# Optimization experiments

Hardware: AMD Instinct MI355X
Metric: run time of the kernel (lower is better)

The kernel has to match this reference:

```python
import jax, jax.numpy as jnp
import numpy as np

# ---- config (matches init_kwargs) ----
B, NP, DIM, HEADS, DH, NDIM = 32, 576, 512, 8, 64, 16
N = NP + 1                 # seq len incl cls token = 577
INNER = HEADS * DH         # 512


def setup_inputs() -> dict:
    key = jax.random.key(0)
    ks = jax.random.split(key, 11)
    D2 = 2 * DIM  # bidirectional EMA doubles kernel dim
    return {
        "x": jax.random.normal(ks[0], (B, N, DIM), jnp.float32),
        "W_qk": jax.random.normal(ks[1], (DIM, 2 * INNER), jnp.float32) / np.float32(np.sqrt(DIM)),
        "W_v": jax.random.normal(ks[2], (DIM, INNER), jnp.float32) / np.float32(np.sqrt(DIM)),
        "W_out": jax.random.normal(ks[3], (INNER, DIM), jnp.float32) / np.float32(np.sqrt(INNER)),
        "b_out": jnp.zeros((DIM,), jnp.float32),
        "rel_bias": jax.random.normal(ks[4], (2 * N - 1,), jnp.float32) * 0.02,
        "ema_delta": jax.random.normal(ks[5], (D2, NDIM, 1), jnp.float32),
        "ema_alpha": jax.random.normal(ks[6], (D2, NDIM, 1), jnp.float32),
        "ema_beta": jax.random.normal(ks[7], (D2, NDIM, 1), jnp.float32) * 0.5,
        "ema_gamma": jax.random.normal(ks[8], (D2, NDIM), jnp.float32) * 0.5,
        "ema_omega": jax.random.normal(ks[9], (DIM,), jnp.float32),
    }


def _ema_move(x, delta, alpha, beta, gamma, omega):
    """Bidirectional MultiHeadEMA (MEGA) via FFT convolution. x: (B, L, D)."""
    b, L, d = x.shape
    scale = jnp.asarray(np.sqrt(1.0 / NDIM), x.dtype)
    p = jax.nn.sigmoid(delta)                      # (2D, N, 1)
    q = 1.0 - p * jax.nn.sigmoid(alpha)            # (2D, N, 1), in (0,1)
    vander = jnp.arange(L, dtype=x.dtype)[None, None, :] * jnp.log(q)  # (2D, N, L)
    kern = (p * beta) * jnp.exp(vander)            # (2D, N, L)
    k = jnp.einsum('dnl,dn->dl', kern, gamma * scale)  # (2D, L)
    k1, k2 = k[:d], k[d:]
    # combined bidirectional kernel, length 2L-1
    kk = jnp.pad(k1, ((0, 0), (L - 1, 0))) + jnp.pad(k2[:, ::-1], ((0, 0), (0, L - 1)))
    xt = jnp.pad(x.transpose(0, 2, 1), ((0, 0), (0, 0), (L - 1, 0)))  # (B, D, 2L-1)
    fft_len = 2 * L - 1
    nfft = 2 * fft_len
    out = jnp.fft.irfft(jnp.fft.rfft(xt, n=nfft) * jnp.fft.rfft(kk, n=nfft)[None], n=nfft)
    s = 2 * L - 2
    out = out[..., s:s + L].transpose(0, 2, 1).astype(x.dtype)  # (B, L, D)
    return jax.nn.silu(out + x * omega)


def _rel_pos_bias(rb, seq_len):
    """RelativePositionalBias (MEGA): (2*N-1,) param -> (seq_len, seq_len) bias."""
    max_pos = N
    bvec = rb[max_pos - seq_len: max_pos + seq_len - 1]   # (2*seq_len-1,)
    t = jnp.pad(bvec, (0, seq_len))
    t = jnp.tile(t, seq_len)[:-seq_len].reshape(seq_len, 3 * seq_len - 2)
    r = (2 * seq_len - 1) // 2
    return t[:, r:t.shape[1] - r]


def reference(x, W_qk, W_v, W_out, b_out, rel_bias,
              ema_delta, ema_alpha, ema_beta, ema_gamma, ema_omega):
    b, n, _ = x.shape
    cls_tok = x[:, :1]
    moved = _ema_move(x[:, 1:], ema_delta, ema_alpha, ema_beta, ema_gamma, ema_omega)
    xm = jnp.concatenate([cls_tok, moved], axis=1)        # (B, N, DIM)
    q, k = jnp.split(xm @ W_qk, 2, axis=-1)
    v = xm @ W_v                                          # smooth_v_as_well=True

    def heads(t):
        return t.reshape(b, n, HEADS, DH).transpose(0, 2, 1, 3)  # (B, H, N, DH)

    q, k, v = heads(q), heads(k), heads(v)
    dots = jnp.einsum('bhid,bhjd->bhij', q, k) * (DH ** -0.5)
    attn = jax.nn.softmax(dots, axis=-1)
    attn = attn + _rel_pos_bias(rel_bias, n)[None, None]  # bias added AFTER softmax
    out = jnp.einsum('bhij,bhjd->bhid', attn, v)
    out = out.transpose(0, 2, 1, 3).reshape(b, n, INNER)
    return out @ W_out + b_out
```

## Files before the change

### kernel.cpp

```cpp
#include <hip/hip_runtime.h>

typedef unsigned short ushort;

typedef __bf16 bf16x8 __attribute__((ext_vector_type(8)));
typedef float  f32x4  __attribute__((ext_vector_type(4)));
typedef unsigned short u16x8 __attribute__((ext_vector_type(8)));
typedef unsigned short u16x4 __attribute__((ext_vector_type(4)));
typedef unsigned int   u32x2 __attribute__((ext_vector_type(2)));

static constexpr int BB   = 32;
static constexpr int NN   = 577;
static constexpr int LL   = 576;
static constexpr int DIMC = 512;
static constexpr int BN   = BB * NN;

static constexpr size_t SZ_WQKVT = 1536ull * 512 * 2;
static constexpr size_t SZ_WOUTT = 512ull * 512 * 2;
static constexpr size_t SZ_QK    = (size_t)BN * 1024 * 2;
static constexpr size_t SZ_V     = (size_t)BN * 512 * 2;
static constexpr size_t SZ_VT    = 256ull * 64 * 640 * 2;
static constexpr size_t OFF_WQKVT = 0;
static constexpr size_t OFF_WOUTT = OFF_WQKVT + SZ_WQKVT;
static constexpr size_t OFF_QTAB  = OFF_WOUTT + SZ_WOUTT;
static constexpr size_t OFF_CTAB  = OFF_QTAB + 65536;
static constexpr size_t OFF_QK    = OFF_CTAB + 65536;
static constexpr size_t OFF_V     = OFF_QK + SZ_QK;
static constexpr size_t OFF_REGION= OFF_V + SZ_V;
static constexpr size_t OFF_XM    = OFF_REGION;
static constexpr size_t OFF_VT    = OFF_REGION;
static constexpr size_t OFF_AO    = OFF_REGION + SZ_VT;
static constexpr size_t WS_NEEDED = OFF_AO + SZ_V;

__device__ __forceinline__ ushort bf16bits(float f) {
  unsigned int u = __builtin_bit_cast(unsigned int, f);
  u = (u + 0x7fffu + ((u >> 16) & 1u)) >> 16;
  return (ushort)u;
}
__device__ __forceinline__ float sigmoidf_(float z) { return 1.f / (1.f + __expf(-z)); }
__device__ __forceinline__ float siluf(float z)     { return z / (1.f + __expf(-z)); }

__global__ __launch_bounds__(256) void k_prep(
    const float* __restrict__ delta, const float* __restrict__ alpha,
    const float* __restrict__ beta,  const float* __restrict__ gamma,
    const float* __restrict__ Wqk,   const float* __restrict__ Wv,
    const float* __restrict__ Wout,
    float* __restrict__ qtab, float* __restrict__ ctab,
    ushort* __restrict__ Wqkvt, ushort* __restrict__ Woutt)
{
  int idx = blockIdx.x * 256 + threadIdx.x;
  if (idx < 16384) {
    float p = sigmoidf_(delta[idx]);
    float q = 1.f - p * sigmoidf_(alpha[idx]);
    qtab[idx] = q;
    ctab[idx] = p * beta[idx] * gamma[idx] * 0.25f;
  }
  int i2 = idx - 16384;
  if (i2 >= 0 && i2 < 1536 * 512) {
    int n = i2 >> 9, k = i2 & 511;
    float w = (n < 1024) ? Wqk[k * 1024 + n] : Wv[k * 512 + (n - 1024)];
    Wqkvt[i2] = bf16bits(w);
  }
  int i3 = i2 - 1536 * 512;
  if (i3 >= 0 && i3 < 512 * 512) {
    int n = i3 >> 9, k = i3 & 511;
    Woutt[i3] = bf16bits(Wout[k * 512 + n]);
  }
}

__global__ __launch_bounds__(64) void k_ema_scan(
    const float* __restrict__ x, const float* __restrict__ qtab,
    const float* __restrict__ ctab, float* __restrict__ y1, float* __restrict__ y2)
{
  const int bx = blockIdx.x;
  const int b  = blockIdx.y;
  if (bx < 8) {
    const int d = bx * 64 + threadIdx.x;
    float q[16], c[16], h[16];
    #pragma unroll
    for (int n = 0; n < 16; ++n) { q[n] = qtab[d*16+n]; c[n] = ctab[d*16+n]; h[n] = 0.f; }
    const float* xp = x  + ((size_t)b * NN + 1) * DIMC + d;
    float*       yp = y1 + ((size_t)b * LL)     * DIMC + d;
    float xn[8];
    #pragma unroll
    for (int u = 0; u < 8; ++u) xn[u] = xp[u * DIMC];
    for (int blk = 0; blk < 72; ++blk) {
      float xv[8];
      #pragma unroll
      for (int u = 0; u < 8; ++u) xv[u] = xn[u];
      if (blk < 71) {
        #pragma unroll
        for (int u = 0; u < 8; ++u) xn[u] = xp[((blk + 1) * 8 + u) * DIMC];
      }
      #pragma unroll
      for (int u = 0; u < 8; ++u) {
        float xx = xv[u], y = 0.f;
        #pragma unroll
        for (int n = 0; n < 16; ++n) { h[n] = fmaf(q[n], h[n], xx); y = fmaf(c[n], h[n], y); }
        yp[(blk * 8 + u) * DIMC] = y;
      }
    }
  } else {
    const int d = (bx - 8) * 64 + threadIdx.x;
    float q[16], c[16], g[16];
    #pragma unroll
    for (int n = 0; n < 16; ++n) { q[n] = qtab[(d+512)*16+n]; c[n] = ctab[(d+512)*16+n]; g[n] = 0.f; }
    const float* xp = x  + ((size_t)b * NN + 1) * DIMC + d;
    float*       yp = y2 + ((size_t)b * LL)     * DIMC + d;
    float xn[8];
    #pragma unroll
    for (int u = 0; u < 8; ++u) xn[u] = xp[(568 + u) * DIMC];
    for (int blk = 71; blk >= 0; --blk) {
      float xv[8];
      #pragma unroll
      for (int u = 0; u < 8; ++u) xv[u] = xn[u];
      if (blk > 0) {
        #pragma unroll
        for (int u = 0; u < 8; ++u) xn[u] = xp[((blk - 1) * 8 + u) * DIMC];
      }
      #pragma unroll
      for (int u = 7; u >= 0; --u) {
        float xx = xv[u], y = 0.f;
        #pragma unroll
        for (int n = 0; n < 16; ++n) { g[n] = fmaf(q[n], g[n], xx); y = fmaf(c[n], g[n], y); }
        yp[(blk * 8 + u) * DIMC] = y;
      }
    }
  }
}

__global__ __launch_bounds__(256) void k_ema_comb(
    const float* __restrict__ x, const float* __restrict__ y1,
    const float* __restrict__ y2, const float* __restrict__ omega,
    ushort* __restrict__ xm)
{
  size_t v = (size_t)blockIdx.x * 256 + threadIdx.x;
  size_t e = v * 4;
  int n = (int)(e >> 9);
  int d = (int)(e & 511);
  int b = n / 577;
  int i = n - b * 577;
  f32x4 xv = *(const f32x4*)(x + e);
  u16x4 o;
  if (i == 0) {
    #pragma unroll
    for (int k = 0; k < 4; ++k) o[k] = bf16bits(xv[k]);
  } else {
    size_t ey = ((size_t)b * LL + (i - 1)) * DIMC + d;
    f32x4 a  = *(const f32x4*)(y1 + ey);
    f32x4 c2 = *(const f32x4*)(y2 + ey);
    f32x4 om = *(const f32x4*)(omega + d);
    #pragma unroll
    for (int k = 0; k < 4; ++k) o[k] = bf16bits(siluf(a[k] + c2[k] + xv[k] * om[k]));
  }
  *(u16x4*)(xm + e) = o;
}

__global__ __launch_bounds__(256) void k_qkv(
    const ushort* __restrict__ A, const ushort* __restrict__ Bt,
    ushort* __restrict__ qk, ushort* __restrict__ v)
{
  __shared__ alignas(16) ushort lA[128 * 40];
  __shared__ alignas(16) ushort lB[128 * 40];
  const int tid = threadIdx.x, wv = tid >> 6, lane = tid & 63;
  const int quad = lane >> 4, c16 = lane & 15;
  const int fid = blockIdx.y * 12 + blockIdx.x;
  const int xcd = fid & 7, ord = fid >> 3;
  const int wg  = (xcd < 4 ? xcd * 218 : 872 + (xcd - 4) * 217) + ord;
  const int row0 = (wg / 12) * 128, n0 = (wg % 12) * 128;
  const int wm = (wv >> 1) * 64, wn = (wv & 1) * 64;
  f32x4 z4 = {0.f, 0.f, 0.f, 0.f};
  f32x4 acc[4][4];
  #pragma unroll
  for (int mi = 0; mi < 4; ++mi)
    #pragma unroll
    for (int ni = 0; ni < 4; ++ni) acc[mi][ni] = z4;

  for (int kt = 0; kt < 16; ++kt) {
    const int k0 = kt * 32;
    u16x8 sa[2], sb[2];
    #pragma unroll
    for (int it = 0; it < 2; ++it) {
      int ch = it * 256 + tid;
      int r = ch >> 2, cc = ch & 3;
      int grow = row0 + r; if (grow > BN - 1) grow = BN - 1;
      sa[it] = *(const u16x8*)(A + (size_t)grow * 512 + k0 + cc * 8);
      sb[it] = *(const u16x8*)(Bt + (size_t)(n0 + r) * 512 + k0 + cc * 8);
    }
    __syncthreads();
    #pragma unroll
    for (int it = 0; it < 2; ++it) {
      int ch = it * 256 + tid;
      int r = ch >> 2, cc = ch & 3;
      *(u16x8*)(lA + r * 40 + cc * 8) = sa[it];
      *(u16x8*)(lB + r * 40 + cc * 8) = sb[it];
    }
    __syncthreads();
    bf16x8 af[4], bfv[4];
    #pragma unroll
    for (int mi = 0; mi < 4; ++mi)
      af[mi] = *(const bf16x8*)(lA + (wm + mi * 16 + c16) * 40 + quad * 8);
    #pragma unroll
    for (int ni = 0; ni < 4; ++ni)
      bfv[ni] = *(const bf16x8*)(lB + (wn + ni * 16 + c16) * 40 + quad * 8);
    #pragma unroll
    for (int mi = 0; mi < 4; ++mi)
      #pragma unroll
      for (int ni = 0; ni < 4; ++ni)
        acc[mi][ni] = __builtin_amdgcn_mfma_f32_16x16x32_bf16(af[mi], bfv[ni], acc[mi][ni], 0, 0, 0);
  }
  const bool isv = (n0 >= 1024);
  const float osc = (n0 < 512) ? 0.125f : 1.0f;
  #pragma unroll
  for (int mi = 0; mi < 4; ++mi) {
    #pragma unroll
    for (int r = 0; r < 4; ++r) {
      int grow = row0 + wm + mi * 16 + quad * 4 + r;
      if (grow < BN) {
        #pragma unroll
        for (int ni = 0; ni < 4; ++ni) {
          int col = n0 + wn + ni * 16 + c16;
          ushort vb = bf16bits(acc[mi][ni][r] * osc);
          if (!isv) qk[(size_t)grow * 1024 + col] = vb;
          else      v[(size_t)grow * 512 + (col - 1024)] = vb;
        }
      }
    }
  }
}

__global__ __launch_bounds__(256) void k_vtrans(
    const ushort* __restrict__ v, ushort* __restrict__ vt)
{
  __shared__ alignas(16) ushort lt[64 * 72];
  const int tid = threadIdx.x;
  const int bh = blockIdx.y, b = bh >> 3, h = bh & 7;
  const int j0 = blockIdx.x * 64;
  #pragma unroll
  for (int pass = 0; pass < 2; ++pass) {
    int cch = pass * 256 + tid;
    int jl = cch >> 3, cc = cch & 7;
    int gj = j0 + jl;
    u16x8 val = {0, 0, 0, 0, 0, 0, 0, 0};
    if (gj < 577) val = *(const u16x8*)(v + ((size_t)(b * NN + gj)) * 512 + h * 64 + cc * 8);
    *(u16x8*)(lt + jl * 72 + cc * 8) = val;
  }
  __syncthreads();
  #pragma unroll
  for (int pass = 0; pass < 2; ++pass) {
    int cch = pass * 256 + tid;
    int dh = cch >> 3, jc = cch & 7;
    u16x8 o;
    #pragma unroll
    for (int e = 0; e < 8; ++e) o[e] = lt[(jc * 8 + e) * 72 + dh];
    *(u16x8*)(vt + ((size_t)(bh * 64 + dh)) * 640 + j0 + jc * 8) = o;
  }
}

__global__ __launch_bounds__(256) void k_fattn(
    const ushort* __restrict__ qk, const ushort* __restrict__ vt,
    const float* __restrict__ relb, ushort* __restrict__ ao)
{
  __shared__ alignas(16) ushort lk[64 * 64];
  __shared__ alignas(16) ushort lv[64 * 64];
  __shared__ alignas(16) ushort lp[128 * 64];
  __shared__ ushort lbias16[1280];
  const int tid = threadIdx.x, wv = tid >> 6, lane = tid & 63;
  const int quad = lane >> 4, c16 = lane & 15;
  const int bh = blockIdx.x, b = bh >> 3, h = bh & 7;
  const int i0 = blockIdx.y * 128, wm = wv * 32;
  for (int t = tid; t < 1280; t += 256) {
    int idx = t - 64;
    lbias16[t] = (idx >= 0 && idx < 1153) ? bf16bits(relb[idx]) : (ushort)0;
  }
  bf16x8 aq[2][2];
  #pragma unroll
  for (int ms = 0; ms < 2; ++ms) {
    int gi = i0 + wm + ms * 16 + c16; if (gi > 576) gi = 576;
    const ushort* qp = qk + ((size_t)(b * NN + gi)) * 1024 + h * 64;
    #pragma unroll
    for (int kk = 0; kk < 2; ++kk)
      aq[ms][kk] = *(const bf16x8*)(qp + (kk * 4 + quad) * 8);
  }
  const int s_r = tid >> 3, s_c = tid & 7;
  const ushort* kbase = qk + ((size_t)b * NN) * 1024 + 512 + h * 64 + s_c * 8;
  const ushort* vbase = vt + ((size_t)bh * 64) * 640 + s_c * 8;

  float lsum[2] = {0.f, 0.f};
  f32x4 z4 = {0.f, 0.f, 0.f, 0.f};
  f32x4 accp[2][4], accb[2][4];
  #pragma unroll
  for (int ms = 0; ms < 2; ++ms)
    #pragma unroll
    for (int ns = 0; ns < 4; ++ns) { accp[ms][ns] = z4; accb[ms][ns] = z4; }

  u16x8 sk[2], sv[2];
  #pragma unroll
  for (int it = 0; it < 2; ++it) {
    int r = it * 32 + s_r;
    sk[it] = *(const u16x8*)(kbase + (size_t)r * 1024);
    sv[it] = *(const u16x8*)(vbase + (size_t)r * 640);
  }

  for (int jt = 0; jt < 10; ++jt) {
    __syncthreads();
    #pragma unroll
    for (int it = 0; it < 2; ++it) {
      int r = it * 32 + s_r;
      int pc = (s_c ^ (r & 7)) * 8;
      *(u16x8*)(lk + r * 64 + pc) = sk[it];
      *(u16x8*)(lv + r * 64 + pc) = sv[it];
    }
    __syncthreads();
    #pragma unroll
    for (int ms = 0; ms < 2; ++ms) {
      f32x4 dacc[4] = {z4, z4, z4, z4};
      #pragma unroll
      for (int kk = 0; kk < 2; ++kk) {
        const int ck = kk * 4 + quad;
        #pragma unroll
        for (int ns = 0; ns < 4; ++ns) {
          const int row = ns * 16 + c16;
          bf16x8 bk = *(const bf16x8*)(lk + row * 64 + ((ck ^ (row & 7)) * 8));
          dacc[ns] = __builtin_amdgcn_mfma_f32_16x16x32_bf16(bk, aq[ms][kk], dacc[ns], 0, 0, 0);
        }
      }
      const int irow = wm + ms * 16 + c16;
      const int xr = irow & 7;
      #pragma unroll
      for (int ns = 0; ns < 4; ++ns) {
        float ex[4];
        #pragma unroll
        for (int r = 0; r < 4; ++r) {
          float e = __expf(dacc[ns][r]);
          if (jt == 9 && (ns * 16 + quad * 4 + r) >= 1) e = 0.f;
          ex[r] = e;
        }
        lsum[ms] += (ex[0] + ex[1]) + (ex[2] + ex[3]);
        unsigned int p0 = (unsigned int)bf16bits(ex[0]) | ((unsigned int)bf16bits(ex[1]) << 16);
        unsigned int p1 = (unsigned int)bf16bits(ex[2]) | ((unsigned int)bf16bits(ex[3]) << 16);
        u32x2 pw = {p0, p1};
        const int lc = ns * 2 + (quad >> 1);
        *(u32x2*)(lp + irow * 64 + ((lc ^ xr) * 8) + (quad & 1) * 4) = pw;
      }
    }
    __syncthreads();
    if (jt < 9) {
      const int j0n = (jt + 1) * 64;
      #pragma unroll
      for (int it = 0; it < 2; ++it) {
        int r = it * 32 + s_r;
        int gj = j0n + r; if (gj > 576) gj = 576;
        sk[it] = *(const u16x8*)(kbase + (size_t)gj * 1024);
        sv[it] = *(const u16x8*)(vbase + (size_t)r * 640 + j0n);
      }
    }
    const int j0 = jt * 64;
    #pragma unroll
    for (int kk = 0; kk < 2; ++kk) {
      const int ck = kk * 4 + quad;
      bf16x8 ap[2], ab[2];
      #pragma unroll
      for (int ms = 0; ms < 2; ++ms) {
        const int row = wm + ms * 16 + c16;
        ap[ms] = *(const bf16x8*)(lp + row * 64 + ((ck ^ (row & 7)) * 8));
        u16x8 abu;
        const int base = 64 + 576 + j0 + kk * 32 + quad * 8 - (i0 + row);
        #pragma unroll
        for (int e = 0; e < 8; ++e) abu[e] = lbias16[base + e];
        ab[ms] = __builtin_bit_cast(bf16x8, abu);
      }
      #pragma unroll
      for (int ns = 0; ns < 4; ++ns) {
        const int row = ns * 16 + c16;
        bf16x8 bV = *(const bf16x8*)(lv + row * 64 + ((ck ^ (row & 7)) * 8));
        #pragma unroll
        for (int ms = 0; ms < 2; ++ms) {
          accp[ms][ns] = __builtin_amdgcn_mfma_f32_16x16x32_bf16(ap[ms], bV, accp[ms][ns], 0, 0, 0);
          accb[ms][ns] = __builtin_amdgcn_mfma_f32_16x16x32_bf16(ab[ms], bV, accb[ms][ns], 0, 0, 0);
        }
      }
    }
  }
  float tot[2];
  #pragma unroll
  for (int ms = 0; ms < 2; ++ms) {
    float t = lsum[ms];
    t += __shfl_xor(t, 16);
    t += __shfl_xor(t, 32);
    tot[ms] = t;
  }
  #pragma unroll
  for (int ms = 0; ms < 2; ++ms) {
    #pragma unroll
    for (int r = 0; r < 4; ++r) {
      float li = 1.f / __shfl(tot[ms], quad * 4 + r);
      int ii = i0 + wm + ms * 16 + quad * 4 + r;
      if (ii < 577) {
        #pragma unroll
        for (int ns = 0; ns < 4; ++ns)
          ao[((size_t)(b * NN + ii)) * 512 + h * 64 + ns * 16 + c16] =
              bf16bits(accp[ms][ns][r] * li + accb[ms][ns][r]);
      }
    }
  }
}

__global__ __launch_bounds__(256) void k_out(
    const ushort* __restrict__ A, const ushort* __restrict__ Bt,
    const float* __restrict__ bout, float* __restrict__ out)
{
  __shared__ alignas(16) ushort lA[128 * 40];
  __shared__ alignas(16) ushort lB[128 * 40];
  const int tid = threadIdx.x, wv = tid >> 6, lane = tid & 63;
  const int quad = lane >> 4, c16 = lane & 15;
  const int row0 = blockIdx.y * 128, n0 = blockIdx.x * 128;
  const int wm = (wv >> 1) * 64, wn = (wv & 1) * 64;
  f32x4 z4 = {0.f, 0.f, 0.f, 0.f};
  f32x4 acc[4][4];
  #pragma unroll
  for (int mi = 0; mi < 4; ++mi)
    #pragma unroll
    for (int ni = 0; ni < 4; ++ni) acc[mi][ni] = z4;

  for (int kt = 0; kt < 16; ++kt) {
    const int k0 = kt * 32;
    u16x8 sa[2], sb[2];
    #pragma unroll
    for (int it = 0; it < 2; ++it) {
      int ch = it * 256 + tid;
      int r = ch >> 2, cc = ch & 3;
      int grow = row0 + r; if (grow > BN - 1) grow = BN - 1;
      sa[it] = *(const u16x8*)(A + (size_t)grow * 512 + k0 + cc * 8);
      sb[it] = *(const u16x8*)(Bt + (size_t)(n0 + r) * 512 + k0 + cc * 8);
    }
    __syncthreads();
    #pragma unroll
    for (int it = 0; it < 2; ++it) {
      int ch = it * 256 + tid;
      int r = ch >> 2, cc = ch & 3;
      *(u16x8*)(lA + r * 40 + cc * 8) = sa[it];
      *(u16x8*)(lB + r * 40 + cc * 8) = sb[it];
    }
    __syncthreads();
    bf16x8 af[4], bfv[4];
    #pragma unroll
    for (int mi = 0; mi < 4; ++mi)
      af[mi] = *(const bf16x8*)(lA + (wm + mi * 16 + c16) * 40 + quad * 8);
    #pragma unroll
    for (int ni = 0; ni < 4; ++ni)
      bfv[ni] = *(const bf16x8*)(lB + (wn + ni * 16 + c16) * 40 + quad * 8);
    #pragma unroll
    for (int mi = 0; mi < 4; ++mi)
      #pragma unroll
      for (int ni = 0; ni < 4; ++ni)
        acc[mi][ni] = __builtin_amdgcn_mfma_f32_16x16x32_bf16(af[mi], bfv[ni], acc[mi][ni], 0, 0, 0);
  }
  #pragma unroll
  for (int mi = 0; mi < 4; ++mi) {
    #pragma unroll
    for (int r = 0; r < 4; ++r) {
      int grow = row0 + wm + mi * 16 + quad * 4 + r;
      if (grow < BN) {
        #pragma unroll
        for (int ni = 0; ni < 4; ++ni) {
          int col = n0 + wn + ni * 16 + c16;
          out[(size_t)grow * 512 + col] = acc[mi][ni][r] + bout[col];
        }
      }
    }
  }
}

extern "C" void kernel_launch(void* const* d_in, const int* in_sizes, int n_in,
                              void* d_out, int out_size, void* d_ws, size_t ws_size,
                              hipStream_t stream) {
  (void)in_sizes; (void)n_in; (void)out_size;
  if (ws_size < WS_NEEDED) return;
  const float* x    = (const float*)d_in[0];
  const float* Wqk  = (const float*)d_in[1];
  const float* Wv   = (const float*)d_in[2];
  const float* Wout = (const float*)d_in[3];
  const float* bout = (const float*)d_in[4];
  const float* relb = (const float*)d_in[5];
  const float* edel = (const float*)d_in[6];
  const float* ealp = (const float*)d_in[7];
  const float* ebet = (const float*)d_in[8];
  const float* egam = (const float*)d_in[9];
  const float* eome = (const float*)d_in[10];

  char* ws = (char*)d_ws;
  ushort* Wqkvt = (ushort*)(ws + OFF_WQKVT);
  ushort* Woutt = (ushort*)(ws + OFF_WOUTT);
  float*  qtab  = (float*)(ws + OFF_QTAB);
  float*  ctab  = (float*)(ws + OFF_CTAB);
  ushort* qkb   = (ushort*)(ws + OFF_QK);
  ushort* vb    = (ushort*)(ws + OFF_V);
  ushort* xm    = (ushort*)(ws + OFF_XM);
  ushort* vtb   = (ushort*)(ws + OFF_VT);
  ushort* aob   = (ushort*)(ws + OFF_AO);
  float*  outp  = (float*)d_out;
  float*  y1    = outp;
  float*  y2    = (float*)(ws + OFF_QK);

  k_prep<<<dim3(4160), dim3(256), 0, stream>>>(edel, ealp, ebet, egam, Wqk, Wv, Wout,
                                               qtab, ctab, Wqkvt, Woutt);
  k_ema_scan<<<dim3(16, 32), dim3(64), 0, stream>>>(x, qtab, ctab, y1, y2);
  k_ema_comb<<<dim3(9232), dim3(256), 0, stream>>>(x, y1, y2, eome, xm);
  k_qkv<<<dim3(12, 145), dim3(256), 0, stream>>>(xm, Wqkvt, qkb, vb);
  k_vtrans<<<dim3(10, 256), dim3(256), 0, stream>>>(vb, vtb);
  k_fattn<<<dim3(256, 5), dim3(256), 0, stream>>>(qkb, vtb, relb, aob);
  k_out<<<dim3(4, 145), dim3(256), 0, stream>>>(aob, Woutt, bout, outp);
}
```

Measured before the change: 356.8 us.

## Split EMA recurrence into chunked three-phase parallel scan

Replaces the single sequential EMA scan kernel (512 blocks of 64 threads, each walking 576 steps) with a three-phase chunked scan. The first phase computes per-chunk end states over 7 chunks of 72 steps, the middle kernel propagates carries across chunks using q^72, and the third phase reruns each chunk from its carried-in state and emits outputs. This raises parallelism 8x so more of the GPU is busy, at the cost of two extra launches, re-reading x and extra state traffic. Chunk states are stored in the attention-output workspace region.

```diff
diff --git a/kernel.cpp b/kernel.cpp
--- a/kernel.cpp
+++ b/kernel.cpp
@@ -29,6 +29,7 @@
 static constexpr size_t OFF_XM    = OFF_REGION;
 static constexpr size_t OFF_VT    = OFF_REGION;
 static constexpr size_t OFF_AO    = OFF_REGION + SZ_VT;
+static constexpr size_t OFF_ST    = OFF_AO;
 static constexpr size_t WS_NEEDED = OFF_AO + SZ_V;
 
 __device__ __forceinline__ ushort bf16bits(float f) {
@@ -67,27 +68,117 @@
   }
 }
 
-__global__ __launch_bounds__(64) void k_ema_scan(
+
+__global__ __launch_bounds__(64) void k_ema_p1(
     const float* __restrict__ x, const float* __restrict__ qtab,
-    const float* __restrict__ ctab, float* __restrict__ y1, float* __restrict__ y2)
-{
-  const int bx = blockIdx.x;
-  const int b  = blockIdx.y;
-  if (bx < 8) {
-    const int d = bx * 64 + threadIdx.x;
+    float* __restrict__ st)
+{
+  const int gx = blockIdx.x, cy = blockIdx.y, b = blockIdx.z;
+  if (gx < 8) {
+    const int d = gx * 64 + threadIdx.x;
+    float q[16], h[16];
+    #pragma unroll
+    for (int n = 0; n < 16; ++n) { q[n] = qtab[d*16+n]; h[n] = 0.f; }
+    const float* xp = x + ((size_t)b * NN + 1) * DIMC + d;
+    const int blo = cy * 9;
+    float xn[8];
+    #pragma unroll
+    for (int u = 0; u < 8; ++u) xn[u] = xp[(blo * 8 + u) * DIMC];
+    for (int blk = blo; blk < blo + 9; ++blk) {
+      float xv[8];
+      #pragma unroll
+      for (int u = 0; u < 8; ++u) xv[u] = xn[u];
+      if (blk < blo + 8) {
+        #pragma unroll
+        for (int u = 0; u < 8; ++u) xn[u] = xp[((blk + 1) * 8 + u) * DIMC];
+      }
+      #pragma unroll
+      for (int u = 0; u < 8; ++u) {
+        float xx = xv[u];
+        #pragma unroll
+        for (int n = 0; n < 16; ++n) h[n] = fmaf(q[n], h[n], xx);
+      }
+    }
+    float* sp = st + (((size_t)b * 8 + cy) * 16) * 512 + d;
+    #pragma unroll
+    for (int n = 0; n < 16; ++n) sp[n * 512] = h[n];
+  } else {
+    const int d = (gx - 8) * 64 + threadIdx.x;
+    float q[16], g[16];
+    #pragma unroll
+    for (int n = 0; n < 16; ++n) { q[n] = qtab[(d+512)*16+n]; g[n] = 0.f; }
+    const float* xp = x + ((size_t)b * NN + 1) * DIMC + d;
+    const int blo = (7 - cy) * 9;
+    float xn[8];
+    #pragma unroll
+    for (int u = 0; u < 8; ++u) xn[u] = xp[((blo + 8) * 8 + u) * DIMC];
+    for (int blk = blo + 8; blk >= blo; --blk) {
+      float xv[8];
+      #pragma unroll
+      for (int u = 0; u < 8; ++u) xv[u] = xn[u];
+      if (blk > blo) {
+        #pragma unroll
+        for (int u = 0; u < 8; ++u) xn[u] = xp[((blk - 1) * 8 + u) * DIMC];
+      }
+      #pragma unroll
+      for (int u = 7; u >= 0; --u) {
+        float xx = xv[u];
+        #pragma unroll
+        for (int n = 0; n < 16; ++n) g[n] = fmaf(q[n], g[n], xx);
+      }
+    }
+    float* sp = st + (((size_t)(32 + b) * 8 + cy) * 16) * 512 + d;
+    #pragma unroll
+    for (int n = 0; n < 16; ++n) sp[n * 512] = g[n];
+  }
+}
+
+__global__ __launch_bounds__(256) void k_ema_mid(
+    const float* __restrict__ qtab, float* __restrict__ st)
+{
+  int idx = blockIdx.x * 256 + threadIdx.x;
+  int d = idx & 511;
+  int rest = idx >> 9;
+  int n = rest & 15;
+  int db = rest >> 4;
+  int dir = db >> 5;
+  float q = qtab[(((size_t)dir << 9) + d) * 16 + n];
+  float q2 = q * q, q4 = q2 * q2, q8 = q4 * q4;
+  float q16 = q8 * q8, q32 = q16 * q16, q64 = q32 * q32;
+  float qL = q64 * q8;
+  float h = 0.f;
+  float* sp = st + ((size_t)db * 128 + n) * 512 + d;
+  #pragma unroll
+  for (int c = 0; c < 8; ++c) {
+    float tmp = (c < 7) ? sp[c * 8192] : 0.f;
+    sp[c * 8192] = h;
+    h = fmaf(qL, h, tmp);
+  }
+}
+
+__global__ __launch_bounds__(64) void k_ema_p3(
+    const float* __restrict__ x, const float* __restrict__ qtab,
+    const float* __restrict__ ctab, const float* __restrict__ st,
+    float* __restrict__ y1, float* __restrict__ y2)
+{
+  const int gx = blockIdx.x, cy = blockIdx.y, b = blockIdx.z;
+  if (gx < 8) {
+    const int d = gx * 64 + threadIdx.x;
     float q[16], c[16], h[16];
-    #pragma unroll
-    for (int n = 0; n < 16; ++n) { q[n] = qtab[d*16+n]; c[n] = ctab[d*16+n]; h[n] = 0.f; }
+    const float* sp = st + (((size_t)b * 8 + cy) * 16) * 512 + d;
+    #pragma unroll
+    for (int n = 0; n < 16; ++n) { q[n] = qtab[d*16+n]; c[n] = ctab[d*16+n]; h[n] = sp[n*512]; }
     const float* xp = x  + ((size_t)b * NN + 1) * DIMC + d;
     float*       yp = y1 + ((size_t)b * LL)     * DIMC + d;
+    const int blo = cy * 9;
     float xn[8];
     #pragma unroll
-    for (int u = 0; u < 8; ++u) xn[u] = xp[u * DIMC];
-    for (int blk = 0; blk < 72; ++blk) {
+    for (int u = 0; u < 8; ++u) xn[u] = xp[(blo * 8 + u) * DIMC];
+    for (int blk = blo; blk < blo + 9; ++blk) {
       float xv[8];
       #pragma unroll
       for (int u = 0; u < 8; ++u) xv[u] = xn[u];
-      if (blk < 71) {
+      if (blk < blo + 8) {
         #pragma unroll
         for (int u = 0; u < 8; ++u) xn[u] = xp[((blk + 1) * 8 + u) * DIMC];
       }
@@ -100,20 +191,22 @@
       }
     }
   } else {
-    const int d = (bx - 8) * 64 + threadIdx.x;
+    const int d = (gx - 8) * 64 + threadIdx.x;
     float q[16], c[16], g[16];
-    #pragma unroll
-    for (int n = 0; n < 16; ++n) { q[n] = qtab[(d+512)*16+n]; c[n] = ctab[(d+512)*16+n]; g[n] = 0.f; }
+    const float* sp = st + (((size_t)(32 + b) * 8 + cy) * 16) * 512 + d;
+    #pragma unroll
+    for (int n = 0; n < 16; ++n) { q[n] = qtab[(d+512)*16+n]; c[n] = ctab[(d+512)*16+n]; g[n] = sp[n*512]; }
     const float* xp = x  + ((size_t)b * NN + 1) * DIMC + d;
     float*       yp = y2 + ((size_t)b * LL)     * DIMC + d;
+    const int blo = (7 - cy) * 9;
     float xn[8];
     #pragma unroll
-    for (int u = 0; u < 8; ++u) xn[u] = xp[(568 + u) * DIMC];
-    for (int blk = 71; blk >= 0; --blk) {
+    for (int u = 0; u < 8; ++u) xn[u] = xp[((blo + 8) * 8 + u) * DIMC];
+    for (int blk = blo + 8; blk >= blo; --blk) {
       float xv[8];
       #pragma unroll
       for (int u = 0; u < 8; ++u) xv[u] = xn[u];
-      if (blk > 0) {
+      if (blk > blo) {
         #pragma unroll
         for (int u = 0; u < 8; ++u) xn[u] = xp[((blk - 1) * 8 + u) * DIMC];
       }
@@ -498,13 +591,16 @@
   ushort* xm    = (ushort*)(ws + OFF_XM);
   ushort* vtb   = (ushort*)(ws + OFF_VT);
   ushort* aob   = (ushort*)(ws + OFF_AO);
+  float*  stf   = (float*)(ws + OFF_ST);
   float*  outp  = (float*)d_out;
   float*  y1    = outp;
   float*  y2    = (float*)(ws + OFF_QK);
 
   k_prep<<<dim3(4160), dim3(256), 0, stream>>>(edel, ealp, ebet, egam, Wqk, Wv, Wout,
                                                qtab, ctab, Wqkvt, Woutt);
-  k_ema_scan<<<dim3(16, 32), dim3(64), 0, stream>>>(x, qtab, ctab, y1, y2);
+  k_ema_p1<<<dim3(16, 7, 32), dim3(64), 0, stream>>>(x, qtab, stf);
+  k_ema_mid<<<dim3(2048), dim3(256), 0, stream>>>(qtab, stf);
+  k_ema_p3<<<dim3(16, 8, 32), dim3(64), 0, stream>>>(x, qtab, ctab, stf, y1, y2);
   k_ema_comb<<<dim3(9232), dim3(256), 0, stream>>>(x, y1, y2, eome, xm);
   k_qkv<<<dim3(12, 145), dim3(256), 0, stream>>>(xm, Wqkvt, qkb, vb);
   k_vtrans<<<dim3(10, 256), dim3(256), 0, stream>>>(vb, vtb);
```

New measurement: 324.6 us. -9.0%, faster.
